# Optimization experiments

Measured on AMD Instinct MI355X. Metric: run time of the kernel, lower is better.

## Reference

```python
import jax, jax.numpy as jnp
import numpy as np

A_DIM, HID, D_EMB, K_CODES, N_TOK = 6, 256, 128, 2048, 65536
BETA = 0.25


def _linear_init(k, fan_in, fan_out):
    lim = 1.0 / np.sqrt(fan_in)
    kw, kb = jax.random.split(k)
    W = jax.random.uniform(kw, (fan_in, fan_out), minval=-lim, maxval=lim, dtype=jnp.float32)
    b = jax.random.uniform(kb, (fan_out,), minval=-lim, maxval=lim, dtype=jnp.float32)
    return W, b


def setup_inputs() -> dict:
    key = jax.random.key(0)
    ks = jax.random.split(key, 8)
    action = jax.random.normal(ks[0], (1, N_TOK, A_DIM), dtype=jnp.float32)
    W_e1, b_e1 = _linear_init(ks[1], A_DIM, HID)
    W_e2, b_e2 = _linear_init(ks[2], HID, HID)
    W_e3, b_e3 = _linear_init(ks[3], HID, D_EMB)
    # codebook init: uniform(-1/K, 1/K) as in the torch module
    emb = jax.random.uniform(ks[4], (K_CODES, D_EMB), minval=-1.0 / K_CODES, maxval=1.0 / K_CODES, dtype=jnp.float32)
    W_d1, b_d1 = _linear_init(ks[5], D_EMB, HID)
    W_d2, b_d2 = _linear_init(ks[6], HID, HID)
    W_d3, b_d3 = _linear_init(ks[7], HID, A_DIM)
    return dict(action=action,
                W_e1=W_e1, b_e1=b_e1, W_e2=W_e2, b_e2=b_e2, W_e3=W_e3, b_e3=b_e3,
                emb=emb,
                W_d1=W_d1, b_d1=b_d1, W_d2=W_d2, b_d2=b_d2, W_d3=W_d3, b_d3=b_d3)


def reference(action, W_e1, b_e1, W_e2, b_e2, W_e3, b_e3, emb,
              W_d1, b_d1, W_d2, b_d2, W_d3, b_d3):
    sg = jax.lax.stop_gradient
    # encoder MLP; note original code does encoder(action)[0] -> [N, D]
    h = jax.nn.relu(action @ W_e1 + b_e1)
    h = jax.nn.relu(h @ W_e2 + b_e2)
    enc = (h @ W_e3 + b_e3)[0]                         # [N, D]
    # squared-distance to codebook: [N, K]
    dist = (jnp.sum(enc ** 2, axis=1, keepdims=True)
            + jnp.sum(emb ** 2, axis=1)
            - 2.0 * enc @ emb.T)
    idx = jnp.argmin(dist, axis=1)                     # [N]
    one_hot = jax.nn.one_hot(idx, emb.shape[0], dtype=enc.dtype)  # [N, K]
    q = one_hot @ emb                                  # [N, D]
    commitment_loss = jnp.mean((sg(q) - enc) ** 2)
    embedding_loss = jnp.mean((q - sg(enc)) ** 2)
    vq_loss = BETA * commitment_loss + embedding_loss
    # straight-through estimator
    q_st = enc + sg(q - enc)
    # decoder MLP
    d = jax.nn.relu(q_st @ W_d1 + b_d1)
    d = jax.nn.relu(d @ W_d2 + b_d2)
    recons = jnp.tanh(d @ W_d3 + b_d3)                 # [N, A]
    recons_loss = jnp.mean((recons - action[0]) ** 2)
    total = recons_loss + vq_loss
    return jnp.stack([total, recons_loss, vq_loss])
```

## Files before the change

### kernel.cpp

```cpp
#include <hip/hip_runtime.h>
#include <stdint.h>

typedef unsigned short u16;
typedef float f32x4 __attribute__((ext_vector_type(4)));
typedef short short8 __attribute__((ext_vector_type(8)));
typedef unsigned uint4v __attribute__((ext_vector_type(4)));

enum { NT = 65536, KC = 2048, D = 128, H = 256, A_DIM = 6 };

__device__ __forceinline__ u16 f2bf(float f) {
    union { float f; unsigned u; } x; x.f = f;
    unsigned r = x.u + 0x7FFFu + ((x.u >> 16) & 1u);
    return (u16)(r >> 16);
}
__device__ __forceinline__ float bf2f(u16 u) {
    union { unsigned u; float f; } x; x.u = ((unsigned)u) << 16;
    return x.f;
}

typedef __attribute__((address_space(1))) void gvoid;
typedef __attribute__((address_space(3))) void lvoid;
__device__ __forceinline__ void gload_lds16(const void* g, void* l) {
    __builtin_amdgcn_global_load_lds((gvoid*)g, (lvoid*)l, 16, 0, 0);
}

__global__ void prep(const float* __restrict__ W_e2, const float* __restrict__ W_e3,
                     const float* __restrict__ W_d1, const float* __restrict__ W_d2,
                     const float* __restrict__ emb,
                     u16* __restrict__ We2T, u16* __restrict__ We3T,
                     u16* __restrict__ Wd1T, u16* __restrict__ Wd2T,
                     u16* __restrict__ emb_bf, float* __restrict__ norm2,
                     float* __restrict__ sums) {
    int b = blockIdx.x, t = threadIdx.x;
    if (b == 0 && t < 2) sums[t] = 0.f;
    if (b < 256)       { int e = b * 256 + t;          int i = e >> 8, j = e & 255; We2T[j * 256 + i] = f2bf(W_e2[e]); }
    else if (b < 384)  { int e = (b - 256) * 256 + t;  int i = e >> 7, j = e & 127; We3T[j * 256 + i] = f2bf(W_e3[e]); }
    else if (b < 512)  { int e = (b - 384) * 256 + t;  int i = e >> 8, j = e & 255; Wd1T[j * 128 + i] = f2bf(W_d1[e]); }
    else if (b < 768)  { int e = (b - 512) * 256 + t;  int i = e >> 8, j = e & 255; Wd2T[j * 256 + i] = f2bf(W_d2[e]); }
    else if (b < 1792) { int e = (b - 768) * 256 + t;  emb_bf[e] = f2bf(emb[e]); }
    else {
        int lane = t & 63, w = t >> 6;
        int r = (b - 1792) * 4 + w;
        float v0 = emb[(size_t)r * D + lane];
        float v1 = emb[(size_t)r * D + 64 + lane];
        float s = v0 * v0 + v1 * v1;
#pragma unroll
        for (int off = 32; off; off >>= 1) s += __shfl_xor(s, off);
        if (lane == 0) norm2[r] = s;
    }
}

__global__ __launch_bounds__(256) void enc1(const float* __restrict__ act, const float* __restrict__ W,
                                            const float* __restrict__ b, u16* __restrict__ h1) {
    const int gid = blockIdx.x * 256 + threadIdx.x;
    const int row = gid >> 5;
    const int col0 = (gid & 31) << 3;
    float x[A_DIM];
#pragma unroll
    for (int i = 0; i < A_DIM; i++) x[i] = act[(size_t)row * A_DIM + i];
    float s[8];
#pragma unroll
    for (int c = 0; c < 8; c++) s[c] = b[col0 + c];
#pragma unroll
    for (int i = 0; i < A_DIM; i++) {
        float xi = x[i];
#pragma unroll
        for (int c = 0; c < 8; c++) s[c] = fmaf(xi, W[i * H + col0 + c], s[c]);
    }
    uint4v o;
#pragma unroll
    for (int c2 = 0; c2 < 4; c2++)
        o[c2] = (unsigned)f2bf(fmaxf(s[c2 * 2], 0.f)) | ((unsigned)f2bf(fmaxf(s[c2 * 2 + 1], 0.f)) << 16);
    *(uint4v*)&h1[(size_t)row * H + col0] = o;
}

__global__ __launch_bounds__(256) void enc23_fused(
    const u16* __restrict__ h1g,
    const u16* __restrict__ We2T, const float* __restrict__ b2,
    const u16* __restrict__ We3T, const float* __restrict__ b3,
    u16* __restrict__ encb) {
    __shared__ __align__(16) u16 hA[64 * 256];
    __shared__ __align__(16) u16 sB[256 * 64];
    const int t = threadIdx.x, lane = t & 63, w = t >> 6;
    const int l15 = lane & 15, khalf = lane >> 4;
    const int row0 = blockIdx.x * 64;
#pragma unroll
    for (int p = 0; p < 8; p++) {
        int db = (p * 256 + t) * 16;
        int r = db >> 9;
        int col = ((db & 511) ^ ((r & 7) << 4)) >> 1;
        gload_lds16(h1g + (size_t)(row0 + r) * H + col, (char*)hA + db);
    }
    int sbDst[8], sbRow[8], sbCol[8];
#pragma unroll
    for (int p = 0; p < 8; p++) {
        int db = (p * 256 + t) * 16;
        int r = db >> 7;
        sbDst[p] = db; sbRow[p] = r;
        sbCol[p] = ((db & 127) ^ ((r & 7) << 4)) >> 1;
    }
    const int kbase = khalf * 8;
    f32x4 acc[4][4] = {};
    for (int kst = 0; kst < 4; kst++) {
        if (kst) __syncthreads();
        const int k0 = kst * 64;
#pragma unroll
        for (int p = 0; p < 8; p++)
            gload_lds16(We2T + (size_t)sbRow[p] * H + k0 + sbCol[p], (char*)sB + sbDst[p]);
        __syncthreads();
#pragma unroll
        for (int ks = 0; ks < 2; ks++) {
            const int k = k0 + ks * 32 + kbase;
            const int kb = (ks * 32 + kbase) << 1;
            short8 av[4], bv[4];
#pragma unroll
            for (int m = 0; m < 4; m++) {
                int rA = m * 16 + l15;
                av[m] = *(const short8*)((const char*)hA + ((rA << 9) | ((k << 1) ^ ((rA & 7) << 4))));
            }
#pragma unroll
            for (int n = 0; n < 4; n++) {
                int rB = w * 64 + n * 16 + l15;
                bv[n] = *(const short8*)((const char*)sB + ((rB << 7) | (kb ^ ((rB & 7) << 4))));
            }
#pragma unroll
            for (int m = 0; m < 4; m++)
#pragma unroll
                for (int n = 0; n < 4; n++)
                    acc[m][n] = __builtin_amdgcn_mfma_f32_16x16x32_bf16(av[m], bv[n], acc[m][n], 0, 0, 0);
        }
    }
    __syncthreads();
#pragma unroll
    for (int n = 0; n < 4; n++) {
        int col = w * 64 + n * 16 + l15;
        float bs = b2[col];
#pragma unroll
        for (int m = 0; m < 4; m++)
#pragma unroll
            for (int j = 0; j < 4; j++) {
                int row = m * 16 + khalf * 4 + j;
                float v = fmaxf(acc[m][n][j] + bs, 0.f);
                *(u16*)((char*)hA + ((row << 9) | ((col << 1) ^ ((row & 7) << 4)))) = f2bf(v);
            }
    }
    __syncthreads();
    f32x4 acc2[4][2] = {};
    for (int kst = 0; kst < 4; kst++) {
        if (kst) __syncthreads();
        const int k0 = kst * 64;
#pragma unroll
        for (int p = 0; p < 4; p++)
            gload_lds16(We3T + (size_t)sbRow[p] * H + k0 + sbCol[p], (char*)sB + sbDst[p]);
        __syncthreads();
#pragma unroll
        for (int ks = 0; ks < 2; ks++) {
            const int k = k0 + ks * 32 + kbase;
            const int kb = (ks * 32 + kbase) << 1;
            short8 av[4], bv[2];
#pragma unroll
            for (int m = 0; m < 4; m++) {
                int rA = m * 16 + l15;
                av[m] = *(const short8*)((const char*)hA + ((rA << 9) | ((k << 1) ^ ((rA & 7) << 4))));
            }
#pragma unroll
            for (int n = 0; n < 2; n++) {
                int rB = w * 32 + n * 16 + l15;
                bv[n] = *(const short8*)((const char*)sB + ((rB << 7) | (kb ^ ((rB & 7) << 4))));
            }
#pragma unroll
            for (int m = 0; m < 4; m++)
#pragma unroll
                for (int n = 0; n < 2; n++)
                    acc2[m][n] = __builtin_amdgcn_mfma_f32_16x16x32_bf16(av[m], bv[n], acc2[m][n], 0, 0, 0);
        }
    }
    __syncthreads();
#pragma unroll
    for (int n = 0; n < 2; n++) {
        int col = w * 32 + n * 16 + l15;
        float bs = b3[col];
#pragma unroll
        for (int m = 0; m < 4; m++)
#pragma unroll
            for (int j = 0; j < 4; j++) {
                int row = m * 16 + khalf * 4 + j;
                ((u16*)sB)[row * 128 + col] = f2bf(acc2[m][n][j] + bs);
            }
    }
    __syncthreads();
#pragma unroll
    for (int p = 0; p < 4; p++) {
        int db = (p * 256 + t) * 16;
        *(uint4v*)((char*)(encb + (size_t)row0 * D) + db) = *(const uint4v*)((const char*)sB + db);
    }
}

__global__ __launch_bounds__(256) void dec_fused(
    const u16* __restrict__ emb_bf, const int* __restrict__ idxbuf,
    const u16* __restrict__ Wd1T, const float* __restrict__ bd1,
    const u16* __restrict__ Wd2T, const float* __restrict__ bd2,
    const float* __restrict__ W3, float* __restrict__ part) {
    __shared__ __align__(16) u16 qA[64 * 128];
    __shared__ __align__(16) u16 hA[64 * 256];
    __shared__ __align__(16) u16 sB[256 * 64];
    const int t = threadIdx.x, lane = t & 63, w = t >> 6;
    const int l15 = lane & 15, khalf = lane >> 4;
    const int row0 = blockIdx.x * 64;
#pragma unroll
    for (int p = 0; p < 4; p++) {
        int db = (p * 256 + t) * 16;
        int r = (p << 4) + (t >> 4);
        int col = ((db & 255) ^ ((r & 7) << 4)) >> 1;
        int kidx = idxbuf[row0 + r];
        gload_lds16(emb_bf + (size_t)kidx * D + col, (char*)qA + db);
    }
    int sbDst[8], sbRow[8], sbCol[8];
#pragma unroll
    for (int p = 0; p < 8; p++) {
        int db = (p * 256 + t) * 16;
        int r = db >> 7;
        sbDst[p] = db; sbRow[p] = r;
        sbCol[p] = ((db & 127) ^ ((r & 7) << 4)) >> 1;
    }
    const int kbase = khalf * 8;
    f32x4 acc[4][4] = {};
    for (int kst = 0; kst < 2; kst++) {
        if (kst) __syncthreads();
        const int k0 = kst * 64;
#pragma unroll
        for (int p = 0; p < 8; p++)
            gload_lds16(Wd1T + (size_t)sbRow[p] * D + k0 + sbCol[p], (char*)sB + sbDst[p]);
        __syncthreads();
#pragma unroll
        for (int ks = 0; ks < 2; ks++) {
            const int k = k0 + ks * 32 + kbase;
            const int kb = (ks * 32 + kbase) << 1;
            short8 av[4], bv[4];
#pragma unroll
            for (int m = 0; m < 4; m++) {
                int rA = m * 16 + l15;
                av[m] = *(const short8*)((const char*)qA + ((rA << 8) | ((k << 1) ^ ((rA & 7) << 4))));
            }
#pragma unroll
            for (int n = 0; n < 4; n++) {
                int rB = w * 64 + n * 16 + l15;
                bv[n] = *(const short8*)((const char*)sB + ((rB << 7) | (kb ^ ((rB & 7) << 4))));
            }
#pragma unroll
            for (int m = 0; m < 4; m++)
#pragma unroll
                for (int n = 0; n < 4; n++)
                    acc[m][n] = __builtin_amdgcn_mfma_f32_16x16x32_bf16(av[m], bv[n], acc[m][n], 0, 0, 0);
        }
    }
#pragma unroll
    for (int n = 0; n < 4; n++) {
        int col = w * 64 + n * 16 + l15;
        float bs = bd1[col];
#pragma unroll
        for (int m = 0; m < 4; m++)
#pragma unroll
            for (int j = 0; j < 4; j++) {
                int row = m * 16 + khalf * 4 + j;
                float v = fmaxf(acc[m][n][j] + bs, 0.f);
                *(u16*)((char*)hA + ((row << 9) | ((col << 1) ^ ((row & 7) << 4)))) = f2bf(v);
            }
    }
    __syncthreads();
    f32x4 acc2[4][4] = {};
    for (int kst = 0; kst < 4; kst++) {
        if (kst) __syncthreads();
        const int k0 = kst * 64;
#pragma unroll
        for (int p = 0; p < 8; p++)
            gload_lds16(Wd2T + (size_t)sbRow[p] * H + k0 + sbCol[p], (char*)sB + sbDst[p]);
        __syncthreads();
#pragma unroll
        for (int ks = 0; ks < 2; ks++) {
            const int k = k0 + ks * 32 + kbase;
            const int kb = (ks * 32 + kbase) << 1;
            short8 av[4], bv[4];
#pragma unroll
            for (int m = 0; m < 4; m++) {
                int rA = m * 16 + l15;
                av[m] = *(const short8*)((const char*)hA + ((rA << 9) | ((k << 1) ^ ((rA & 7) << 4))));
            }
#pragma unroll
            for (int n = 0; n < 4; n++) {
                int rB = w * 64 + n * 16 + l15;
                bv[n] = *(const short8*)((const char*)sB + ((rB << 7) | (kb ^ ((rB & 7) << 4))));
            }
#pragma unroll
            for (int m = 0; m < 4; m++)
#pragma unroll
                for (int n = 0; n < 4; n++)
                    acc2[m][n] = __builtin_amdgcn_mfma_f32_16x16x32_bf16(av[m], bv[n], acc2[m][n], 0, 0, 0);
        }
    }
    float W3r[4][A_DIM], bs[4];
#pragma unroll
    for (int n = 0; n < 4; n++) {
        int col = w * 64 + n * 16 + l15;
        bs[n] = bd2[col];
#pragma unroll
        for (int j = 0; j < A_DIM; j++) W3r[n][j] = W3[col * A_DIM + j];
    }
    float* ps = part + (size_t)w * NT * A_DIM;
#pragma unroll
    for (int m = 0; m < 4; m++) {
#pragma unroll
        for (int j = 0; j < 4; j++) {
            int row = row0 + m * 16 + khalf * 4 + j;
            float p6[A_DIM] = {};
#pragma unroll
            for (int n = 0; n < 4; n++) {
                float v = fmaxf(acc2[m][n][j] + bs[n], 0.f);
#pragma unroll
                for (int jj = 0; jj < A_DIM; jj++) p6[jj] = fmaf(v, W3r[n][jj], p6[jj]);
            }
#pragma unroll
            for (int off = 1; off < 16; off <<= 1)
#pragma unroll
                for (int jj = 0; jj < A_DIM; jj++) p6[jj] += __shfl_xor(p6[jj], off);
            if (l15 == 0) {
#pragma unroll
                for (int jj = 0; jj < A_DIM; jj++) ps[(size_t)row * A_DIM + jj] = p6[jj];
            }
        }
    }
}

__global__ __launch_bounds__(256) void head_final(const float* __restrict__ part, const float* __restrict__ b3,
                                                  const float* __restrict__ act, float* __restrict__ sums) {
    __shared__ float sred[4];
    const int t = threadIdx.x, lane = t & 63, w = t >> 6;
    const int n = blockIdx.x * 256 + t;
    float s = 0.f;
#pragma unroll
    for (int j = 0; j < A_DIM; j++) {
        float v = b3[j];
#pragma unroll
        for (int sl = 0; sl < 4; sl++) v += part[(size_t)sl * NT * A_DIM + (size_t)n * A_DIM + j];
        float r = tanhf(v);
        float df = r - act[(size_t)n * A_DIM + j];
        s += df * df;
    }
#pragma unroll
    for (int off = 32; off; off >>= 1) s += __shfl_xor(s, off);
    if (lane == 0) sred[w] = s;
    __syncthreads();
    if (t == 0) atomicAdd(&sums[1], sred[0] + sred[1] + sred[2] + sred[3]);
}

__global__ __launch_bounds__(256) void vq_dist(const u16* __restrict__ enc_bf, const u16* __restrict__ emb_bf,
                                               const float* __restrict__ norm2,
                                               int* __restrict__ idxbuf, float* __restrict__ sums) {
    __shared__ u16 sA[128 * 128];
    __shared__ u16 sB[128 * 128];
    __shared__ float sN[KC];
    __shared__ unsigned sKey[128];
    __shared__ float svq[4];
    const int t = threadIdx.x, lane = t & 63, w = t >> 6, wr = w >> 1, wc = w & 1;
    const int row0 = blockIdx.x * 128;
    int srow[8], sdst[8], scol[8];
#pragma unroll
    for (int p = 0; p < 8; p++) {
        int db = (p * 256 + t) * 16;
        int row = db >> 8;
        srow[p] = row; sdst[p] = db;
        scol[p] = ((db & 255) ^ ((row & 7) << 4)) >> 1;
    }
#pragma unroll
    for (int p = 0; p < 8; p++) gload_lds16(enc_bf + (size_t)(row0 + srow[p]) * D + scol[p], (char*)sA + sdst[p]);
#pragma unroll
    for (int p = 0; p < 8; p++) gload_lds16(emb_bf + (size_t)srow[p] * D + scol[p], (char*)sB + sdst[p]);
    for (int i = t; i < KC; i += 256) sN[i] = norm2[i] + 1.0f;
    const int ra = wr * 64 + (lane & 15), rb = wc * 64 + (lane & 15);
    const int kbase = (lane >> 4) * 8;
    int boff[4][4];
#pragma unroll
    for (int m = 0; m < 4; m++)
#pragma unroll
        for (int ks = 0; ks < 4; ks++) {
            int rB = rb + m * 16;
            int kb = (ks * 32 + kbase) << 1;
            boff[m][ks] = (rB << 8) | (kb ^ ((rB & 7) << 4));
        }
    __syncthreads();
    short8 av[4][4];
#pragma unroll
    for (int m = 0; m < 4; m++)
#pragma unroll
        for (int ks = 0; ks < 4; ks++) {
            int rA = ra + m * 16;
            int kb = (ks * 32 + kbase) << 1;
            av[m][ks] = *(const short8*)((const char*)sA + ((rA << 8) | (kb ^ ((rA & 7) << 4))));
        }
    unsigned minKey[4][4];
#pragma unroll
    for (int m = 0; m < 4; m++)
#pragma unroll
        for (int j = 0; j < 4; j++) minKey[m][j] = 0xFFFFFFFFu;
    for (int ch = 0; ch < 16; ch++) {
        if (ch) {
            __syncthreads();
            const u16* src = emb_bf + (size_t)ch * 128 * D;
#pragma unroll
            for (int p = 0; p < 8; p++) gload_lds16(src + (size_t)srow[p] * D + scol[p], (char*)sB + sdst[p]);
            __syncthreads();
        }
        f32x4 acc[4][4] = {};
#pragma unroll
        for (int ks = 0; ks < 4; ks++) {
            short8 bv[4];
#pragma unroll
            for (int n = 0; n < 4; n++) bv[n] = *(const short8*)((const char*)sB + boff[n][ks]);
#pragma unroll
            for (int m = 0; m < 4; m++)
#pragma unroll
                for (int n = 0; n < 4; n++)
                    acc[m][n] = __builtin_amdgcn_mfma_f32_16x16x32_bf16(av[m][ks], bv[n], acc[m][n], 0, 0, 0);
        }
#pragma unroll
        for (int n = 0; n < 4; n++) {
            int k = ch * 128 + rb + n * 16;
            float nn = sN[k];
#pragma unroll
            for (int m = 0; m < 4; m++)
#pragma unroll
                for (int j = 0; j < 4; j++) {
                    float c = fmaf(acc[m][n][j], -2.f, nn);
                    unsigned key = (__float_as_uint(c) & 0xFFFFF800u) | (unsigned)k;
                    minKey[m][j] = min(minKey[m][j], key);
                }
        }
    }
#pragma unroll
    for (int off = 1; off < 16; off <<= 1) {
#pragma unroll
        for (int m = 0; m < 4; m++)
#pragma unroll
            for (int j = 0; j < 4; j++)
                minKey[m][j] = min(minKey[m][j], (unsigned)__shfl_xor((int)minKey[m][j], off));
    }
    __syncthreads();
    if (wc == 0 && (lane & 15) == 0) {
#pragma unroll
        for (int m = 0; m < 4; m++)
#pragma unroll
            for (int j = 0; j < 4; j++) {
                int row = wr * 64 + m * 16 + (lane >> 4) * 4 + j;
                sKey[row] = minKey[m][j];
            }
    }
    __syncthreads();
    if (wc == 1 && (lane & 15) == 0) {
#pragma unroll
        for (int m = 0; m < 4; m++)
#pragma unroll
            for (int j = 0; j < 4; j++) {
                int row = wr * 64 + m * 16 + (lane >> 4) * 4 + j;
                if (minKey[m][j] < sKey[row]) sKey[row] = minKey[m][j];
            }
    }
    __syncthreads();
    float vql = 0.f;
    if (t < 128) {
        unsigned sk = sKey[t];
        idxbuf[row0 + t] = (int)(sk & 0x7FFu);
        vql = __uint_as_float(sk & 0xFFFFF800u) - 1.0f;
    }
#pragma unroll
    for (int i = 0; i < 8; i++) {
        short8 v = *(const short8*)((const char*)sA + i * 4096 + t * 16);
#pragma unroll
        for (int j = 0; j < 8; j++) { float e = bf2f((u16)v[j]); vql = fmaf(e, e, vql); }
    }
#pragma unroll
    for (int off = 32; off; off >>= 1) vql += __shfl_xor(vql, off);
    if (lane == 0) svq[w] = vql;
    __syncthreads();
    if (t == 0) atomicAdd(&sums[0], svq[0] + svq[1] + svq[2] + svq[3]);
}

__global__ void finalize(const float* __restrict__ sums, float* __restrict__ out) {
    if (threadIdx.x == 0) {
        float vq = 1.25f * sums[0] / (float)(NT * D);
        float rec = sums[1] / (float)(NT * A_DIM);
        out[0] = rec + vq;
        out[1] = rec;
        out[2] = vq;
    }
}

extern "C" void kernel_launch(void* const* d_in, const int* in_sizes, int n_in,
                              void* d_out, int out_size, void* d_ws, size_t ws_size,
                              hipStream_t stream) {
    const float* action = (const float*)d_in[0];
    const float* W_e1 = (const float*)d_in[1];
    const float* b_e1 = (const float*)d_in[2];
    const float* W_e2 = (const float*)d_in[3];
    const float* b_e2 = (const float*)d_in[4];
    const float* W_e3 = (const float*)d_in[5];
    const float* b_e3 = (const float*)d_in[6];
    const float* emb  = (const float*)d_in[7];
    const float* W_d1 = (const float*)d_in[8];
    const float* b_d1 = (const float*)d_in[9];
    const float* W_d2 = (const float*)d_in[10];
    const float* b_d2 = (const float*)d_in[11];
    const float* W_d3 = (const float*)d_in[12];
    const float* b_d3 = (const float*)d_in[13];

    char* ws = (char*)d_ws;
    float* sums  = (float*)ws;
    float* norm2 = (float*)(ws + 256);
    u16* We2T   = (u16*)(ws + 8448);
    u16* We3T   = (u16*)(ws + 139520);
    u16* Wd1T   = (u16*)(ws + 205056);
    u16* Wd2T   = (u16*)(ws + 270592);
    u16* emb_bf = (u16*)(ws + 401664);
    u16* h1     = (u16*)(ws + 925952);
    float* part = (float*)(ws + 925952 + 33554432);
    u16* encb   = (u16*)(ws + 925952 + 67108864);
    int* idxbuf = (int*)(ws + 925952 + 83886080);

    prep<<<2304, 256, 0, stream>>>(W_e2, W_e3, W_d1, W_d2, emb, We2T, We3T, Wd1T, Wd2T, emb_bf, norm2, sums);
    enc1<<<NT * 32 / 256, 256, 0, stream>>>(action, W_e1, b_e1, h1);
    enc23_fused<<<NT / 64, 256, 0, stream>>>(h1, We2T, b_e2, We3T, b_e3, encb);
    vq_dist<<<NT / 128, 256, 0, stream>>>(encb, emb_bf, norm2, idxbuf, sums);
    dec_fused<<<NT / 64, 256, 0, stream>>>(emb_bf, idxbuf, Wd1T, b_d1, Wd2T, b_d2, W_d3, part);
    head_final<<<NT / 256, 256, 0, stream>>>(part, b_d3, action, sums);
    finalize<<<1, 64, 0, stream>>>(sums, (float*)d_out);
}
```

Measured before the change: 142.8 us.

## Fuse first encoder layer and decoder head into neighbouring kernels

The first encoder linear layer (6->256) is now computed inside enc23_fused and written straight into shared memory, so the h1 intermediate no longer goes through global memory. Likewise, the tanh head and reconstruction loss are computed inside dec_fused through a shared-memory slab, which removes the partial-sum buffer and the head_final launch. This saves two kernel launches and roughly 50+ MB of global traffic. In exchange, each block does the small layer-1 FMA work before its first MFMA step, and dec_fused issues one atomic per 64 rows.

```diff
diff --git a/kernel.cpp b/kernel.cpp
--- a/kernel.cpp
+++ b/kernel.cpp
@@ -50,32 +50,8 @@
     }
 }
 
-__global__ __launch_bounds__(256) void enc1(const float* __restrict__ act, const float* __restrict__ W,
-                                            const float* __restrict__ b, u16* __restrict__ h1) {
-    const int gid = blockIdx.x * 256 + threadIdx.x;
-    const int row = gid >> 5;
-    const int col0 = (gid & 31) << 3;
-    float x[A_DIM];
-#pragma unroll
-    for (int i = 0; i < A_DIM; i++) x[i] = act[(size_t)row * A_DIM + i];
-    float s[8];
-#pragma unroll
-    for (int c = 0; c < 8; c++) s[c] = b[col0 + c];
-#pragma unroll
-    for (int i = 0; i < A_DIM; i++) {
-        float xi = x[i];
-#pragma unroll
-        for (int c = 0; c < 8; c++) s[c] = fmaf(xi, W[i * H + col0 + c], s[c]);
-    }
-    uint4v o;
-#pragma unroll
-    for (int c2 = 0; c2 < 4; c2++)
-        o[c2] = (unsigned)f2bf(fmaxf(s[c2 * 2], 0.f)) | ((unsigned)f2bf(fmaxf(s[c2 * 2 + 1], 0.f)) << 16);
-    *(uint4v*)&h1[(size_t)row * H + col0] = o;
-}
-
 __global__ __launch_bounds__(256) void enc23_fused(
-    const u16* __restrict__ h1g,
+    const float* __restrict__ act, const float* __restrict__ W1, const float* __restrict__ b1,
     const u16* __restrict__ We2T, const float* __restrict__ b2,
     const u16* __restrict__ We3T, const float* __restrict__ b3,
     u16* __restrict__ encb) {
@@ -84,13 +60,6 @@
     const int t = threadIdx.x, lane = t & 63, w = t >> 6;
     const int l15 = lane & 15, khalf = lane >> 4;
     const int row0 = blockIdx.x * 64;
-#pragma unroll
-    for (int p = 0; p < 8; p++) {
-        int db = (p * 256 + t) * 16;
-        int r = db >> 9;
-        int col = ((db & 511) ^ ((r & 7) << 4)) >> 1;
-        gload_lds16(h1g + (size_t)(row0 + r) * H + col, (char*)hA + db);
-    }
     int sbDst[8], sbRow[8], sbCol[8];
 #pragma unroll
     for (int p = 0; p < 8; p++) {
@@ -102,17 +71,64 @@
     const int kbase = khalf * 8;
     f32x4 acc[4][4] = {};
     for (int kst = 0; kst < 4; kst++) {
-        if (kst) __syncthreads();
+        if (kst == 0) {
+#pragma unroll
+            for (int p = 0; p < 8; p++)
+                gload_lds16(We2T + (size_t)sbRow[p] * H + sbCol[p], (char*)sB + sbDst[p]);
+            {
+                const int col0h = (t & 31) << 3;
+                const int rbase = (t >> 5) << 3;
+                float W1r[A_DIM][8];
+#pragma unroll
+                for (int i = 0; i < A_DIM; i++) {
+                    f32x4 wa = *(const f32x4*)&W1[i * H + col0h];
+                    f32x4 wb = *(const f32x4*)&W1[i * H + col0h + 4];
+#pragma unroll
+                    for (int c = 0; c < 4; c++) { W1r[i][c] = wa[c]; W1r[i][c + 4] = wb[c]; }
+                }
+                float bv[8];
+                {
+                    f32x4 ba = *(const f32x4*)&b1[col0h];
+                    f32x4 bb = *(const f32x4*)&b1[col0h + 4];
+#pragma unroll
+                    for (int c = 0; c < 4; c++) { bv[c] = ba[c]; bv[c + 4] = bb[c]; }
+                }
+#pragma unroll
+                for (int r8 = 0; r8 < 8; r8++) {
+                    int r = rbase + r8;
+                    float x[A_DIM];
+#pragma unroll
+                    for (int i = 0; i < A_DIM; i++) x[i] = act[(size_t)(row0 + r) * A_DIM + i];
+                    float s[8];
+#pragma unroll
+                    for (int c = 0; c < 8; c++) s[c] = bv[c];
+#pragma unroll
+                    for (int i = 0; i < A_DIM; i++) {
+                        float xi = x[i];
+#pragma unroll
+                        for (int c = 0; c < 8; c++) s[c] = fmaf(xi, W1r[i][c], s[c]);
+                    }
+                    uint4v o;
+#pragma unroll
+                    for (int c2 = 0; c2 < 4; c2++)
+                        o[c2] = (unsigned)f2bf(fmaxf(s[c2 * 2], 0.f)) | ((unsigned)f2bf(fmaxf(s[c2 * 2 + 1], 0.f)) << 16);
+                    *(uint4v*)((char*)hA + ((r << 9) | ((col0h << 1) ^ ((r & 7) << 4)))) = o;
+                }
+            }
+        } else {
+            __syncthreads();
+            const int k0 = kst * 64;
+#pragma unroll
+            for (int p = 0; p < 8; p++)
+                gload_lds16(We2T + (size_t)sbRow[p] * H + k0 + sbCol[p], (char*)sB + sbDst[p]);
+        }
+        __syncthreads();
         const int k0 = kst * 64;
-#pragma unroll
-        for (int p = 0; p < 8; p++)
-            gload_lds16(We2T + (size_t)sbRow[p] * H + k0 + sbCol[p], (char*)sB + sbDst[p]);
-        __syncthreads();
 #pragma unroll
         for (int ks = 0; ks < 2; ks++) {
             const int k = k0 + ks * 32 + kbase;
             const int kb = (ks * 32 + kbase) << 1;
-            short8 av[4], bv[4];
+            short8 av[4], bvv[4];
 #pragma unroll
             for (int m = 0; m < 4; m++) {
                 int rA = m * 16 + l15;
@@ -121,13 +137,13 @@
 #pragma unroll
             for (int n = 0; n < 4; n++) {
                 int rB = w * 64 + n * 16 + l15;
-                bv[n] = *(const short8*)((const char*)sB + ((rB << 7) | (kb ^ ((rB & 7) << 4))));
+                bvv[n] = *(const short8*)((const char*)sB + ((rB << 7) | (kb ^ ((rB & 7) << 4))));
             }
 #pragma unroll
             for (int m = 0; m < 4; m++)
 #pragma unroll
                 for (int n = 0; n < 4; n++)
-                    acc[m][n] = __builtin_amdgcn_mfma_f32_16x16x32_bf16(av[m], bv[n], acc[m][n], 0, 0, 0);
+                    acc[m][n] = __builtin_amdgcn_mfma_f32_16x16x32_bf16(av[m], bvv[n], acc[m][n], 0, 0, 0);
         }
     }
     __syncthreads();
@@ -157,7 +173,7 @@
         for (int ks = 0; ks < 2; ks++) {
             const int k = k0 + ks * 32 + kbase;
             const int kb = (ks * 32 + kbase) << 1;
-            short8 av[4], bv[2];
+            short8 av[4], bvv[2];
 #pragma unroll
             for (int m = 0; m < 4; m++) {
                 int rA = m * 16 + l15;
@@ -166,13 +182,13 @@
 #pragma unroll
             for (int n = 0; n < 2; n++) {
                 int rB = w * 32 + n * 16 + l15;
-                bv[n] = *(const short8*)((const char*)sB + ((rB << 7) | (kb ^ ((rB & 7) << 4))));
+                bvv[n] = *(const short8*)((const char*)sB + ((rB << 7) | (kb ^ ((rB & 7) << 4))));
             }
 #pragma unroll
             for (int m = 0; m < 4; m++)
 #pragma unroll
                 for (int n = 0; n < 2; n++)
-                    acc2[m][n] = __builtin_amdgcn_mfma_f32_16x16x32_bf16(av[m], bv[n], acc2[m][n], 0, 0, 0);
+                    acc2[m][n] = __builtin_amdgcn_mfma_f32_16x16x32_bf16(av[m], bvv[n], acc2[m][n], 0, 0, 0);
         }
     }
     __syncthreads();
@@ -200,7 +216,8 @@
     const u16* __restrict__ emb_bf, const int* __restrict__ idxbuf,
     const u16* __restrict__ Wd1T, const float* __restrict__ bd1,
     const u16* __restrict__ Wd2T, const float* __restrict__ bd2,
-    const float* __restrict__ W3, float* __restrict__ part) {
+    const float* __restrict__ W3, const float* __restrict__ b3,
+    const float* __restrict__ actg, float* __restrict__ sums) {
     __shared__ __align__(16) u16 qA[64 * 128];
     __shared__ __align__(16) u16 hA[64 * 256];
     __shared__ __align__(16) u16 sB[256 * 64];
@@ -236,7 +253,7 @@
         for (int ks = 0; ks < 2; ks++) {
             const int k = k0 + ks * 32 + kbase;
             const int kb = (ks * 32 + kbase) << 1;
-            short8 av[4], bv[4];
+            short8 av[4], bvv[4];
 #pragma unroll
             for (int m = 0; m < 4; m++) {
                 int rA = m * 16 + l15;
@@ -245,13 +262,13 @@
 #pragma unroll
             for (int n = 0; n < 4; n++) {
                 int rB = w * 64 + n * 16 + l15;
-                bv[n] = *(const short8*)((const char*)sB + ((rB << 7) | (kb ^ ((rB & 7) << 4))));
+                bvv[n] = *(const short8*)((const char*)sB + ((rB << 7) | (kb ^ ((rB & 7) << 4))));
             }
 #pragma unroll
             for (int m = 0; m < 4; m++)
 #pragma unroll
                 for (int n = 0; n < 4; n++)
-                    acc[m][n] = __builtin_amdgcn_mfma_f32_16x16x32_bf16(av[m], bv[n], acc[m][n], 0, 0, 0);
+                    acc[m][n] = __builtin_amdgcn_mfma_f32_16x16x32_bf16(av[m], bvv[n], acc[m][n], 0, 0, 0);
         }
     }
 #pragma unroll
@@ -280,7 +297,7 @@
         for (int ks = 0; ks < 2; ks++) {
             const int k = k0 + ks * 32 + kbase;
             const int kb = (ks * 32 + kbase) << 1;
-            short8 av[4], bv[4];
+            short8 av[4], bvv[4];
 #pragma unroll
             for (int m = 0; m < 4; m++) {
                 int rA = m * 16 + l15;
@@ -289,13 +306,13 @@
 #pragma unroll
             for (int n = 0; n < 4; n++) {
                 int rB = w * 64 + n * 16 + l15;
-                bv[n] = *(const short8*)((const char*)sB + ((rB << 7) | (kb ^ ((rB & 7) << 4))));
+                bvv[n] = *(const short8*)((const char*)sB + ((rB << 7) | (kb ^ ((rB & 7) << 4))));
             }
 #pragma unroll
             for (int m = 0; m < 4; m++)
 #pragma unroll
                 for (int n = 0; n < 4; n++)
-                    acc2[m][n] = __builtin_amdgcn_mfma_f32_16x16x32_bf16(av[m], bv[n], acc2[m][n], 0, 0, 0);
+                    acc2[m][n] = __builtin_amdgcn_mfma_f32_16x16x32_bf16(av[m], bvv[n], acc2[m][n], 0, 0, 0);
         }
     }
     float W3r[4][A_DIM], bs[4];
@@ -306,12 +323,13 @@
 #pragma unroll
         for (int j = 0; j < A_DIM; j++) W3r[n][j] = W3[col * A_DIM + j];
     }
-    float* ps = part + (size_t)w * NT * A_DIM;
+    float* slab = (float*)qA;
+    __syncthreads();
 #pragma unroll
     for (int m = 0; m < 4; m++) {
 #pragma unroll
         for (int j = 0; j < 4; j++) {
-            int row = row0 + m * 16 + khalf * 4 + j;
+            int rowl = m * 16 + khalf * 4 + j;
             float p6[A_DIM] = {};
 #pragma unroll
             for (int n = 0; n < 4; n++) {
@@ -325,32 +343,27 @@
                 for (int jj = 0; jj < A_DIM; jj++) p6[jj] += __shfl_xor(p6[jj], off);
             if (l15 == 0) {
 #pragma unroll
-                for (int jj = 0; jj < A_DIM; jj++) ps[(size_t)row * A_DIM + jj] = p6[jj];
-            }
-        }
-    }
-}
-
-__global__ __launch_bounds__(256) void head_final(const float* __restrict__ part, const float* __restrict__ b3,
-                                                  const float* __restrict__ act, float* __restrict__ sums) {
-    __shared__ float sred[4];
-    const int t = threadIdx.x, lane = t & 63, w = t >> 6;
-    const int n = blockIdx.x * 256 + t;
-    float s = 0.f;
-#pragma unroll
-    for (int j = 0; j < A_DIM; j++) {
-        float v = b3[j];
-#pragma unroll
-        for (int sl = 0; sl < 4; sl++) v += part[(size_t)sl * NT * A_DIM + (size_t)n * A_DIM + j];
-        float r = tanhf(v);
-        float df = r - act[(size_t)n * A_DIM + j];
-        s += df * df;
-    }
-#pragma unroll
-    for (int off = 32; off; off >>= 1) s += __shfl_xor(s, off);
-    if (lane == 0) sred[w] = s;
-    __syncthreads();
-    if (t == 0) atomicAdd(&sums[1], sred[0] + sred[1] + sred[2] + sred[3]);
+                for (int jj = 0; jj < A_DIM; jj++) slab[((w << 6) + rowl) * A_DIM + jj] = p6[jj];
+            }
+        }
+    }
+    __syncthreads();
+    if (t < 64) {
+        float s = 0.f;
+        int row = row0 + t;
+#pragma unroll
+        for (int jj = 0; jj < A_DIM; jj++) {
+            float v = b3[jj];
+#pragma unroll
+            for (int sl = 0; sl < 4; sl++) v += slab[((sl << 6) + t) * A_DIM + jj];
+            float r = tanhf(v);
+            float df = r - actg[(size_t)row * A_DIM + jj];
+            s = fmaf(df, df, s);
+        }
+#pragma unroll
+        for (int off = 32; off; off >>= 1) s += __shfl_xor(s, off);
+        if (t == 0) atomicAdd(&sums[1], s);
+    }
 }
 
 __global__ __launch_bounds__(256) void vq_dist(const u16* __restrict__ enc_bf, const u16* __restrict__ emb_bf,
@@ -449,20 +462,20 @@
 #pragma unroll
         for (int m = 0; m < 4; m++)
 #pragma unroll
-            for (int j = 0; j < 4; j++) {
-                int row = wr * 64 + m * 16 + (lane >> 4) * 4 + j;
-                sKey[row] = minKey[m][j];
-            }
+        for (int j = 0; j < 4; j++) {
+            int row = wr * 64 + m * 16 + (lane >> 4) * 4 + j;
+            sKey[row] = minKey[m][j];
+        }
     }
     __syncthreads();
     if (wc == 1 && (lane & 15) == 0) {
 #pragma unroll
         for (int m = 0; m < 4; m++)
 #pragma unroll
-            for (int j = 0; j < 4; j++) {
-                int row = wr * 64 + m * 16 + (lane >> 4) * 4 + j;
-                if (minKey[m][j] < sKey[row]) sKey[row] = minKey[m][j];
-            }
+        for (int j = 0; j < 4; j++) {
+            int row = wr * 64 + m * 16 + (lane >> 4) * 4 + j;
+            if (minKey[m][j] < sKey[row]) sKey[row] = minKey[m][j];
+        }
     }
     __syncthreads();
     float vql = 0.f;
@@ -520,16 +533,12 @@
     u16* Wd1T   = (u16*)(ws + 205056);
     u16* Wd2T   = (u16*)(ws + 270592);
     u16* emb_bf = (u16*)(ws + 401664);
-    u16* h1     = (u16*)(ws + 925952);
-    float* part = (float*)(ws + 925952 + 33554432);
     u16* encb   = (u16*)(ws + 925952 + 67108864);
     int* idxbuf = (int*)(ws + 925952 + 83886080);
 
     prep<<<2304, 256, 0, stream>>>(W_e2, W_e3, W_d1, W_d2, emb, We2T, We3T, Wd1T, Wd2T, emb_bf, norm2, sums);
-    enc1<<<NT * 32 / 256, 256, 0, stream>>>(action, W_e1, b_e1, h1);
-    enc23_fused<<<NT / 64, 256, 0, stream>>>(h1, We2T, b_e2, We3T, b_e3, encb);
+    enc23_fused<<<NT / 64, 256, 0, stream>>>(action, W_e1, b_e1, We2T, b_e2, We3T, b_e3, encb);
     vq_dist<<<NT / 128, 256, 0, stream>>>(encb, emb_bf, norm2, idxbuf, sums);
-    dec_fused<<<NT / 64, 256, 0, stream>>>(emb_bf, idxbuf, Wd1T, b_d1, Wd2T, b_d2, W_d3, part);
-    head_final<<<NT / 256, 256, 0, stream>>>(part, b_d3, action, sums);
+    dec_fused<<<NT / 64, 256, 0, stream>>>(emb_bf, idxbuf, Wd1T, b_d1, Wd2T, b_d2, W_d3, b_d3, action, sums);
     finalize<<<1, 64, 0, stream>>>(sums, (float*)d_out);
 }
```

New measurement: 126.3 us, median of 3. -11.6%, faster.
